# Kernel tuning notes

Measured on AMD Instinct MI355X. Metric: run time of the kernel, lower is better.

The kernel has to match this reference:

```python
import jax, jax.numpy as jnp
import numpy as np

SEARCH_SIZE = 21
BLOCK_SIZE = 4


def _inter_prediction(im1, im2, search_size=SEARCH_SIZE, block_size=BLOCK_SIZE):
    # im1, im2: [B, 1, H, W]; returns [B, 1, H, W]
    B, C, H, W = im1.shape
    p = search_size // 2
    s2 = search_size * search_size
    im2_pad = jnp.pad(im2, ((0, 0), (0, 0), (p, p), (p, p)))
    # All SxS shifted views of im2, stacked on channel dim: [B, S^2, H, W].
    # Channel k = (i, j) row-major corresponds to im2_pad[:, :, i:i+H, j:j+W],
    # matching the torch double loop (note: output is permutation-invariant
    # over shifts anyway since weights are derived from the same tensor).
    nbr = jax.lax.conv_general_dilated_patches(
        im2_pad, (search_size, search_size), (1, 1), 'VALID')
    diff = jnp.abs(im1 - nbr)  # broadcast [B,1,H,W] against [B,S^2,H,W]
    h, w = H // block_size, W // block_size
    # avg_pool2d with kernel=stride=block_size via reshape-mean
    vol = diff.reshape(B, s2, h, block_size, w, block_size).mean(axis=(3, 5))
    idx = jax.nn.softmax(-100.0 * vol, axis=1)  # [B, S^2, h, w]
    # repeat_interleave(block_size) along both spatial dims
    idx_full = jnp.broadcast_to(
        idx[:, :, :, None, :, None],
        (B, s2, h, block_size, w, block_size)).reshape(B, s2, H, W)
    return jnp.sum(idx_full * nbr, axis=1, keepdims=True)


def setup_inputs() -> dict:
    key = jax.random.key(0)
    k1, k2 = jax.random.split(key)
    im1 = jax.random.normal(k1, (2, 1, 256, 256), dtype=jnp.float32)
    im2 = jax.random.normal(k2, (2, 1, 256, 256), dtype=jnp.float32)
    return {"im1": im1, "im2": im2}


def reference(im1, im2):
    return _inter_prediction(im1, im2)
```

## Files before the change

### kernel.cpp

```cpp
#include <hip/hip_runtime.h>
#include <math.h>


typedef float v2f __attribute__((ext_vector_type(2)));

#define HH 256
#define WW 256
#define PAD 10
#define NR 28
#define NC 28
#define CSTR 29
#define LDSN (NC * CSTR)

template <int CTRL>
__device__ __forceinline__ float dppf(float x) {
  return __builtin_bit_cast(
      float, __builtin_amdgcn_update_dpp(0, __builtin_bit_cast(int, x), CTRL,
                                         0xF, 0xF, true));
}

__global__ __launch_bounds__(256, 4) void pred_kernel(
    const float* __restrict__ im1, const float* __restrict__ im2,
    float* __restrict__ out) {
  __shared__ __attribute__((aligned(16))) float win2[LDSN];

  const int tid = threadIdx.x;
  const int T = blockIdx.x;
  const int b = T >> 10;
  const int rem = T & 1023;
  const int tr = rem >> 5;
  const int tc = rem & 31;
  const float* im2b = im2 + b * (HH * WW);

  const int wave = tid >> 6;
  const int lane = tid & 63;
  const int by = tr * 2 + (wave >> 1);
  const int bx = tc * 2 + (wave & 1);

  v2f a2[4][2];
  {
    const float* im1b = im1 + b * (HH * WW) + (by * 4) * WW + bx * 4;
    const float4 r0 = *reinterpret_cast<const float4*>(im1b + 0 * WW);
    const float4 r1 = *reinterpret_cast<const float4*>(im1b + 1 * WW);
    const float4 r2 = *reinterpret_cast<const float4*>(im1b + 2 * WW);
    const float4 r3 = *reinterpret_cast<const float4*>(im1b + 3 * WW);
    a2[0][0] = (v2f){r0.x, r1.x}; a2[1][0] = (v2f){r0.y, r1.y};
    a2[2][0] = (v2f){r0.z, r1.z}; a2[3][0] = (v2f){r0.w, r1.w};
    a2[0][1] = (v2f){r2.x, r3.x}; a2[1][1] = (v2f){r2.y, r3.y};
    a2[2][1] = (v2f){r2.z, r3.z}; a2[3][1] = (v2f){r2.w, r3.w};
  }

  {
    const int gr0 = tr * 8 - PAD;
    const int gc0 = tc * 8 - PAD;
    if (((unsigned)(tr - 2) < 28u) & ((unsigned)(tc - 2) < 28u)) {
      for (int e = tid; e < NR * (NC / 2); e += 256) {
        const int r = e / 14;
        const int c2 = e - r * 14;
        const float2 v = *reinterpret_cast<const float2*>(
            &im2b[(gr0 + r) * WW + (gc0 + 2 * c2)]);
        win2[(2 * c2 + 0) * CSTR + r] = v.x;
        win2[(2 * c2 + 1) * CSTR + r] = v.y;
      }
    } else {
      for (int e = tid; e < NR * (NC / 2); e += 256) {
        const int r = e / 14;
        const int c2 = e - r * 14;
        const int gr = gr0 + r;
        const int gc = gc0 + 2 * c2;
        float2 v = {0.f, 0.f};
        if (((unsigned)gr < HH) & ((unsigned)gc < WW))
          v = *reinterpret_cast<const float2*>(&im2b[gr * WW + gc]);
        win2[(2 * c2 + 0) * CSTR + r] = v.x;
        win2[(2 * c2 + 1) * CSTR + r] = v.y;
      }
    }
  }
  __syncthreads();

  const int i = lane / 3;
  const int j0 = (lane - i * 3) * 7;
  const int ir = i + (wave >> 1) * 4;
  const int jc = j0 + (wave & 1) * 4;
  const int baseIdx = (lane == 63) ? 0 : (jc * CSTR + ir);

  v2f w2[10][2];
#pragma unroll
  for (int c = 0; c < 10; ++c) {
    const float* p = &win2[baseIdx + c * CSTR];
    w2[c][0] = (v2f){p[0], p[1]};
    w2[c][1] = (v2f){p[2], p[3]};
  }

  float sad[7];
#pragma unroll
  for (int t = 0; t < 7; ++t) {
    v2f acc = (v2f){0.f, 0.f};
#pragma unroll
    for (int c = 0; c < 4; ++c) {
#pragma unroll
      for (int rp = 0; rp < 2; ++rp) {
        const v2f d = a2[c][rp] - w2[t + c][rp];
        acc += __builtin_elementwise_max(d, -d);
      }
    }
    sad[t] = acc.x + acc.y;
  }
  if (lane == 63) {
#pragma unroll
    for (int t = 0; t < 7; ++t) sad[t] = 3.0e38f;
  }

  float m;
  {
    const float m0 = fminf(sad[0], sad[1]);
    const float m1 = fminf(sad[2], sad[3]);
    const float m2 = fminf(sad[4], sad[5]);
    m = fminf(fminf(m0, m1), fminf(m2, sad[6]));
  }
  m = fminf(m, dppf<0xB1>(m));
  m = fminf(m, dppf<0x4E>(m));
  m = fminf(m, __shfl_xor(m, 4, 64));
  m = fminf(m, dppf<0x128>(m));
  m = fminf(m, __shfl_xor(m, 16, 64));
  m = fminf(m, __shfl_xor(m, 32, 64));

  const float cc = 9.016844005556021f;
  const float cm = cc * m;
  float l = 0.f;
  v2f o2[4][2];
#pragma unroll
  for (int c = 0; c < 4; ++c)
#pragma unroll
    for (int rp = 0; rp < 2; ++rp) o2[c][rp] = (v2f){0.f, 0.f};
#pragma unroll
  for (int t = 0; t < 7; ++t) {
    const float p = __builtin_amdgcn_exp2f(__builtin_fmaf(-cc, sad[t], cm));
    l += p;
    const v2f pv = (v2f){p, p};
#pragma unroll
    for (int c = 0; c < 4; ++c)
#pragma unroll
      for (int rp = 0; rp < 2; ++rp)
        o2[c][rp] += pv * w2[t + c][rp];
  }

  float o[16];
#pragma unroll
  for (int c = 0; c < 4; ++c)
#pragma unroll
    for (int rp = 0; rp < 2; ++rp) {
      o[(2 * rp + 0) * 4 + c] = o2[c][rp].x;
      o[(2 * rp + 1) * 4 + c] = o2[c][rp].y;
    }

  float r8[8];
  {
    const bool t1 = (lane & 1) != 0;
#pragma unroll
    for (int q = 0; q < 8; ++q) {
      const float send = t1 ? o[q] : o[q + 8];
      const float recv = dppf<0xB1>(send);
      r8[q] = (t1 ? o[q + 8] : o[q]) + recv;
    }
  }
  float r4[4];
  {
    const bool t2 = (lane & 2) != 0;
#pragma unroll
    for (int q = 0; q < 4; ++q) {
      const float send = t2 ? r8[q] : r8[q + 4];
      const float recv = dppf<0x4E>(send);
      r4[q] = (t2 ? r8[q + 4] : r8[q]) + recv;
    }
  }
  float r2[2];
  {
    const bool t8 = (lane & 8) != 0;
#pragma unroll
    for (int q = 0; q < 2; ++q) {
      const float send = t8 ? r4[q] : r4[q + 2];
      const float recv = dppf<0x128>(send);
      r2[q] = (t8 ? r4[q + 2] : r4[q]) + recv;
    }
  }
  float r1;
  {
    const bool t4 = (lane & 4) != 0;
    const float send = t4 ? r2[0] : r2[1];
    const float recv = __shfl_xor(send, 4, 64);
    r1 = (t4 ? r2[1] : r2[0]) + recv;
  }
  r1 += __shfl_xor(r1, 16, 64);
  r1 += __shfl_xor(r1, 32, 64);

  l += dppf<0xB1>(l);
  l += dppf<0x4E>(l);
  l += __shfl_xor(l, 4, 64);
  l += dppf<0x128>(l);
  l += __shfl_xor(l, 16, 64);
  l += __shfl_xor(l, 32, 64);
  const float rinv = __builtin_amdgcn_rcpf(l);

  if (lane < 16) {
    const int dy = ((lane & 1) << 1) | ((lane >> 1) & 1);
    const int dx = ((lane & 8) >> 2) | ((lane & 4) >> 2);
    out[b * (HH * WW) + (by * 4 + dy) * WW + bx * 4 + dx] = r1 * rinv;
  }
}

extern "C" void kernel_launch(void* const* d_in, const int* in_sizes, int n_in,
                              void* d_out, int out_size, void* d_ws, size_t ws_size,
                              hipStream_t stream) {
  const float* im1 = (const float*)d_in[0];
  const float* im2 = (const float*)d_in[1];
  float* out = (float*)d_out;
  const int B = in_sizes[0] / (HH * WW);
  pred_kernel<<<B * 1024, 256, 0, stream>>>(im1, im2, out);
}
```

Before: 62.25 us.

## Process two horizontally adjacent tiles per block reusing a wider LDS window

Each block now covers a 2x4 block region (two tile steps along x) and loads a 28x36 im2 window instead of 28x28, halving the grid. After the first tile is computed, the register window is shifted by 8 columns, reusing two columns and reading eight new ones from LDS, then the second tile is computed. This is meant to cut redundant global loads of the overlapping search halo and per-block launch and sync overhead. The cost is longer per-block serial work and fewer blocks, which lowers parallelism on a 256-CU device.

```diff
diff --git a/kernel.cpp b/kernel.cpp
--- a/kernel.cpp
+++ b/kernel.cpp
@@ -8,9 +8,9 @@
 #define WW 256
 #define PAD 10
 #define NR 28
-#define NC 28
+#define NCW 36
 #define CSTR 29
-#define LDSN (NC * CSTR)
+#define LDSN (NCW * CSTR)
 
 template <int CTRL>
 __device__ __forceinline__ float dppf(float x) {
@@ -19,6 +19,140 @@
                                          0xF, 0xF, true));
 }
 
+__device__ __forceinline__ void load_a2(const float* __restrict__ im1b,
+                                        v2f a2[4][2]) {
+  const float4 r0 = *reinterpret_cast<const float4*>(im1b + 0 * WW);
+  const float4 r1 = *reinterpret_cast<const float4*>(im1b + 1 * WW);
+  const float4 r2 = *reinterpret_cast<const float4*>(im1b + 2 * WW);
+  const float4 r3 = *reinterpret_cast<const float4*>(im1b + 3 * WW);
+  a2[0][0] = (v2f){r0.x, r1.x}; a2[1][0] = (v2f){r0.y, r1.y};
+  a2[2][0] = (v2f){r0.z, r1.z}; a2[3][0] = (v2f){r0.w, r1.w};
+  a2[0][1] = (v2f){r2.x, r3.x}; a2[1][1] = (v2f){r2.y, r3.y};
+  a2[2][1] = (v2f){r2.z, r3.z}; a2[3][1] = (v2f){r2.w, r3.w};
+}
+
+__device__ __forceinline__ void tile_compute(const v2f a2[4][2],
+                                             const v2f w2[10][2],
+                                             float* __restrict__ outb,
+                                             const int lane, const int by,
+                                             const int bx) {
+  float sad[7];
+#pragma unroll
+  for (int t = 0; t < 7; ++t) {
+    v2f acc = (v2f){0.f, 0.f};
+#pragma unroll
+    for (int c = 0; c < 4; ++c) {
+#pragma unroll
+      for (int rp = 0; rp < 2; ++rp) {
+        const v2f d = a2[c][rp] - w2[t + c][rp];
+        acc += __builtin_elementwise_max(d, -d);
+      }
+    }
+    sad[t] = acc.x + acc.y;
+  }
+  if (lane == 63) {
+#pragma unroll
+    for (int t = 0; t < 7; ++t) sad[t] = 3.0e38f;
+  }
+
+  float m;
+  {
+    const float m0 = fminf(sad[0], sad[1]);
+    const float m1 = fminf(sad[2], sad[3]);
+    const float m2 = fminf(sad[4], sad[5]);
+    m = fminf(fminf(m0, m1), fminf(m2, sad[6]));
+  }
+  m = fminf(m, dppf<0xB1>(m));
+  m = fminf(m, dppf<0x4E>(m));
+  m = fminf(m, __shfl_xor(m, 4, 64));
+  m = fminf(m, dppf<0x128>(m));
+  m = fminf(m, __shfl_xor(m, 16, 64));
+  m = fminf(m, __shfl_xor(m, 32, 64));
+
+  const float cc = 9.016844005556021f;
+  const float cm = cc * m;
+  float l = 0.f;
+  v2f o2[4][2];
+#pragma unroll
+  for (int c = 0; c < 4; ++c)
+#pragma unroll
+    for (int rp = 0; rp < 2; ++rp) o2[c][rp] = (v2f){0.f, 0.f};
+#pragma unroll
+  for (int t = 0; t < 7; ++t) {
+    const float p = __builtin_amdgcn_exp2f(__builtin_fmaf(-cc, sad[t], cm));
+    l += p;
+    const v2f pv = (v2f){p, p};
+#pragma unroll
+    for (int c = 0; c < 4; ++c)
+#pragma unroll
+      for (int rp = 0; rp < 2; ++rp)
+        o2[c][rp] += pv * w2[t + c][rp];
+  }
+
+  float o[16];
+#pragma unroll
+  for (int c = 0; c < 4; ++c)
+#pragma unroll
+    for (int rp = 0; rp < 2; ++rp) {
+      o[(2 * rp + 0) * 4 + c] = o2[c][rp].x;
+      o[(2 * rp + 1) * 4 + c] = o2[c][rp].y;
+    }
+
+  float r8[8];
+  {
+    const bool t1 = (lane & 1) != 0;
+#pragma unroll
+    for (int q = 0; q < 8; ++q) {
+      const float send = t1 ? o[q] : o[q + 8];
+      const float recv = dppf<0xB1>(send);
+      r8[q] = (t1 ? o[q + 8] : o[q]) + recv;
+    }
+  }
+  float r4[4];
+  {
+    const bool t2 = (lane & 2) != 0;
+#pragma unroll
+    for (int q = 0; q < 4; ++q) {
+      const float send = t2 ? r8[q] : r8[q + 4];
+      const float recv = dppf<0x4E>(send);
+      r4[q] = (t2 ? r8[q + 4] : r8[q]) + recv;
+    }
+  }
+  float r2[2];
+  {
+    const bool t8 = (lane & 8) != 0;
+#pragma unroll
+    for (int q = 0; q < 2; ++q) {
+      const float send = t8 ? r4[q] : r4[q + 2];
+      const float recv = dppf<0x128>(send);
+      r2[q] = (t8 ? r4[q + 2] : r4[q]) + recv;
+    }
+  }
+  float r1;
+  {
+    const bool t4 = (lane & 4) != 0;
+    const float send = t4 ? r2[0] : r2[1];
+    const float recv = __shfl_xor(send, 4, 64);
+    r1 = (t4 ? r2[1] : r2[0]) + recv;
+  }
+  r1 += __shfl_xor(r1, 16, 64);
+  r1 += __shfl_xor(r1, 32, 64);
+
+  l += dppf<0xB1>(l);
+  l += dppf<0x4E>(l);
+  l += __shfl_xor(l, 4, 64);
+  l += dppf<0x128>(l);
+  l += __shfl_xor(l, 16, 64);
+  l += __shfl_xor(l, 32, 64);
+  const float rinv = __builtin_amdgcn_rcpf(l);
+
+  if (lane < 16) {
+    const int dy = ((lane & 1) << 1) | ((lane >> 1) & 1);
+    const int dx = ((lane & 8) >> 2) | ((lane & 4) >> 2);
+    outb[(by * 4 + dy) * WW + bx * 4 + dx] = r1 * rinv;
+  }
+}
+
 __global__ __launch_bounds__(256, 4) void pred_kernel(
     const float* __restrict__ im1, const float* __restrict__ im2,
     float* __restrict__ out) {
@@ -26,46 +160,38 @@
 
   const int tid = threadIdx.x;
   const int T = blockIdx.x;
-  const int b = T >> 10;
-  const int rem = T & 1023;
-  const int tr = rem >> 5;
-  const int tc = rem & 31;
+  const int b = T >> 9;
+  const int rem = T & 511;
+  const int tr = rem >> 4;
+  const int k = rem & 15;
   const float* im2b = im2 + b * (HH * WW);
+  float* outb = out + b * (HH * WW);
 
   const int wave = tid >> 6;
   const int lane = tid & 63;
   const int by = tr * 2 + (wave >> 1);
-  const int bx = tc * 2 + (wave & 1);
+  const int bxA = 4 * k + (wave & 1);
 
   v2f a2[4][2];
-  {
-    const float* im1b = im1 + b * (HH * WW) + (by * 4) * WW + bx * 4;
-    const float4 r0 = *reinterpret_cast<const float4*>(im1b + 0 * WW);
-    const float4 r1 = *reinterpret_cast<const float4*>(im1b + 1 * WW);
-    const float4 r2 = *reinterpret_cast<const float4*>(im1b + 2 * WW);
-    const float4 r3 = *reinterpret_cast<const float4*>(im1b + 3 * WW);
-    a2[0][0] = (v2f){r0.x, r1.x}; a2[1][0] = (v2f){r0.y, r1.y};
-    a2[2][0] = (v2f){r0.z, r1.z}; a2[3][0] = (v2f){r0.w, r1.w};
-    a2[0][1] = (v2f){r2.x, r3.x}; a2[1][1] = (v2f){r2.y, r3.y};
-    a2[2][1] = (v2f){r2.z, r3.z}; a2[3][1] = (v2f){r2.w, r3.w};
-  }
+  const float* im1base = im1 + b * (HH * WW);
+  load_a2(im1base + (by * 4) * WW + bxA * 4, a2);
 
   {
     const int gr0 = tr * 8 - PAD;
-    const int gc0 = tc * 8 - PAD;
-    if (((unsigned)(tr - 2) < 28u) & ((unsigned)(tc - 2) < 28u)) {
-      for (int e = tid; e < NR * (NC / 2); e += 256) {
-        const int r = e / 14;
-        const int c2 = e - r * 14;
+    const int gc0 = 16 * k - PAD;
+    if (((unsigned)(tr - 2) < 28u) & ((unsigned)(k - 1) < 14u)) {
+      for (int e = tid; e < NR * (NCW / 2); e += 256) {
+        const int r = e / (NCW / 2);
+        const int c2 = e - r * (NCW / 2);
         const float2 v = *reinterpret_cast<const float2*>(
             &im2b[(gr0 + r) * WW + (gc0 + 2 * c2)]);
         win2[(2 * c2 + 0) * CSTR + r] = v.x;
         win2[(2 * c2 + 1) * CSTR + r] = v.y;
       }
     } else {
-      for (int e = tid; e < NR * (NC / 2); e += 256) {
-        const int r = e / 14;
-        const int c2 = e - r * 14;
+      for (int e = tid; e < NR * (NCW / 2); e += 256) {
+        const int r = e / (NCW / 2);
+        const int c2 = e - r * (NCW / 2);
         const int gr = gr0 + r;
         const int gc = gc0 + 2 * c2;
         float2 v = {0.f, 0.f};
@@ -92,121 +218,19 @@
     w2[c][1] = (v2f){p[2], p[3]};
   }
 
-  float sad[7];
-#pragma unroll
-  for (int t = 0; t < 7; ++t) {
-    v2f acc = (v2f){0.f, 0.f};
-#pragma unroll
-    for (int c = 0; c < 4; ++c) {
-#pragma unroll
-      for (int rp = 0; rp < 2; ++rp) {
-        const v2f d = a2[c][rp] - w2[t + c][rp];
-        acc += __builtin_elementwise_max(d, -d);
-      }
-    }
-    sad[t] = acc.x + acc.y;
-  }
-  if (lane == 63) {
-#pragma unroll
-    for (int t = 0; t < 7; ++t) sad[t] = 3.0e38f;
-  }
-
-  float m;
-  {
-    const float m0 = fminf(sad[0], sad[1]);
-    const float m1 = fminf(sad[2], sad[3]);
-    const float m2 = fminf(sad[4], sad[5]);
-    m = fminf(fminf(m0, m1), fminf(m2, sad[6]));
-  }
-  m = fminf(m, dppf<0xB1>(m));
-  m = fminf(m, dppf<0x4E>(m));
-  m = fminf(m, __shfl_xor(m, 4, 64));
-  m = fminf(m, dppf<0x128>(m));
-  m = fminf(m, __shfl_xor(m, 16, 64));
-  m = fminf(m, __shfl_xor(m, 32, 64));
-
-  const float cc = 9.016844005556021f;
-  const float cm = cc * m;
-  float l = 0.f;
-  v2f o2[4][2];
-#pragma unroll
-  for (int c = 0; c < 4; ++c)
-#pragma unroll
-    for (int rp = 0; rp < 2; ++rp) o2[c][rp] = (v2f){0.f, 0.f};
-#pragma unroll
-  for (int t = 0; t < 7; ++t) {
-    const float p = __builtin_amdgcn_exp2f(__builtin_fmaf(-cc, sad[t], cm));
-    l += p;
-    const v2f pv = (v2f){p, p};
-#pragma unroll
-    for (int c = 0; c < 4; ++c)
-#pragma unroll
-      for (int rp = 0; rp < 2; ++rp)
-        o2[c][rp] += pv * w2[t + c][rp];
-  }
-
-  float o[16];
-#pragma unroll
-  for (int c = 0; c < 4; ++c)
-#pragma unroll
-    for (int rp = 0; rp < 2; ++rp) {
-      o[(2 * rp + 0) * 4 + c] = o2[c][rp].x;
-      o[(2 * rp + 1) * 4 + c] = o2[c][rp].y;
-    }
-
-  float r8[8];
-  {
-    const bool t1 = (lane & 1) != 0;
-#pragma unroll
-    for (int q = 0; q < 8; ++q) {
-      const float send = t1 ? o[q] : o[q + 8];
-      const float recv = dppf<0xB1>(send);
-      r8[q] = (t1 ? o[q + 8] : o[q]) + recv;
-    }
-  }
-  float r4[4];
-  {
-    const bool t2 = (lane & 2) != 0;
-#pragma unroll
-    for (int q = 0; q < 4; ++q) {
-      const float send = t2 ? r8[q] : r8[q + 4];
-      const float recv = dppf<0x4E>(send);
-      r4[q] = (t2 ? r8[q + 4] : r8[q]) + recv;
-    }
-  }
-  float r2[2];
-  {
-    const bool t8 = (lane & 8) != 0;
-#pragma unroll
-    for (int q = 0; q < 2; ++q) {
-      const float send = t8 ? r4[q] : r4[q + 2];
-      const float recv = dppf<0x128>(send);
-      r2[q] = (t8 ? r4[q + 2] : r4[q]) + recv;
-    }
-  }
-  float r1;
-  {
-    const bool t4 = (lane & 4) != 0;
-    const float send = t4 ? r2[0] : r2[1];
-    const float recv = __shfl_xor(send, 4, 64);
-    r1 = (t4 ? r2[1] : r2[0]) + recv;
-  }
-  r1 += __shfl_xor(r1, 16, 64);
-  r1 += __shfl_xor(r1, 32, 64);
-
-  l += dppf<0xB1>(l);
-  l += dppf<0x4E>(l);
-  l += __shfl_xor(l, 4, 64);
-  l += dppf<0x128>(l);
-  l += __shfl_xor(l, 16, 64);
-  l += __shfl_xor(l, 32, 64);
-  const float rinv = __builtin_amdgcn_rcpf(l);
-
-  if (lane < 16) {
-    const int dy = ((lane & 1) << 1) | ((lane >> 1) & 1);
-    const int dx = ((lane & 8) >> 2) | ((lane & 4) >> 2);
-    out[b * (HH * WW) + (by * 4 + dy) * WW + bx * 4 + dx] = r1 * rinv;
-  }
+  tile_compute(a2, w2, outb, lane, by, bxA);
+
+  load_a2(im1base + (by * 4) * WW + (bxA + 2) * 4, a2);
+  w2[0][0] = w2[8][0]; w2[0][1] = w2[8][1];
+  w2[1][0] = w2[9][0]; w2[1][1] = w2[9][1];
+#pragma unroll
+  for (int c = 2; c < 10; ++c) {
+    const float* p = &win2[baseIdx + (8 + c) * CSTR];
+    w2[c][0] = (v2f){p[0], p[1]};
+    w2[c][1] = (v2f){p[2], p[3]};
+  }
+
+  tile_compute(a2, w2, outb, lane, by, bxA + 2);
 }
 
 extern "C" void kernel_launch(void* const* d_in, const int* in_sizes, int n_in,
@@ -216,5 +240,5 @@
   const float* im2 = (const float*)d_in[1];
   float* out = (float*)d_out;
   const int B = in_sizes[0] / (HH * WW);
-  pred_kernel<<<B * 1024, 256, 0, stream>>>(im1, im2, out);
-}
+  pred_kernel<<<B * 512, 256, 0, stream>>>(im1, im2, out);
+}
```

Result: no change. 62.67 us (+0.7%).
